# Kernel tuning notes

Hardware: AMD Instinct MI355X
Metric: run time of the kernel (lower is better)

## Reference

```python
import jax, jax.numpy as jnp
import numpy as np

N = 20000      # num nodes (num_words == num_sents, required by residual/linear reuse)
D = 128        # Dw == Ds (original code applies linear_word to both branches)
NE = 640000    # num edges
NEG_SLOPE = 0.2


def gat_conv(x, src, dst, W, a_src, a_dst, bias, num_nodes):
    """PyG GATConv, heads=1, concat=True. Edges are (src -> dst); softmax over
    incoming edges of each dst node."""
    h = x @ W                                   # (N, D_out)
    s_src = h @ a_src                           # (N,) att score per node as source
    s_dst = h @ a_dst                           # (N,) att score per node as target
    e = jax.nn.leaky_relu(s_src[src] + s_dst[dst], NEG_SLOPE)   # (E,)
    # segment softmax over dst
    emax = jax.ops.segment_max(e, dst, num_segments=num_nodes)  # (N,) -inf for empty ok
    ex = jnp.exp(e - emax[dst])                                  # (E,)
    denom = jax.ops.segment_sum(ex, dst, num_segments=num_nodes)
    alpha = ex / (denom[dst] + 1e-16)                            # (E,)
    out = jax.ops.segment_sum(alpha[:, None] * h[src], dst, num_segments=num_nodes)
    return out + bias


def setup_inputs() -> dict:
    key = jax.random.key(0)
    ks = jax.random.split(key, 12)
    Xw = jax.random.normal(ks[0], (N, D), dtype=jnp.float32)
    Xs = jax.random.normal(ks[1], (N, D), dtype=jnp.float32)
    edge_index = jax.random.randint(ks[2], (2, NE), 0, N)
    sc = 0.1
    return {
        "Xw": Xw,
        "Xs": Xs,
        "edge_index": edge_index,
        # gat_sent2word params (in=Ds, out=Dw)
        "W_s2w": jax.random.normal(ks[3], (D, D), dtype=jnp.float32) * sc,
        "a_src_s2w": jax.random.normal(ks[4], (D,), dtype=jnp.float32) * sc,
        "a_dst_s2w": jax.random.normal(ks[5], (D,), dtype=jnp.float32) * sc,
        "b_s2w": jnp.zeros((D,), dtype=jnp.float32),
        # gat_word2sent params (in=Dw, out=Ds)
        "W_w2s": jax.random.normal(ks[6], (D, D), dtype=jnp.float32) * sc,
        "a_src_w2s": jax.random.normal(ks[7], (D,), dtype=jnp.float32) * sc,
        "a_dst_w2s": jax.random.normal(ks[8], (D,), dtype=jnp.float32) * sc,
        "b_w2s": jnp.zeros((D,), dtype=jnp.float32),
        # linear_word (the original forward uses it for BOTH branches)
        "W_lin": jax.random.normal(ks[9], (D, D), dtype=jnp.float32) * sc,
        "b_lin": jnp.zeros((D,), dtype=jnp.float32),
    }


def reference(Xw, Xs, edge_index, W_s2w, a_src_s2w, a_dst_s2w, b_s2w,
              W_w2s, a_src_w2s, a_dst_w2s, b_w2s, W_lin, b_lin):
    num_nodes = Xw.shape[0]
    src, dst = edge_index[0], edge_index[1]
    # sent2word uses E as-is; word2sent uses Erev (flipped pairs)
    temp_word = gat_conv(Xs, src, dst, W_s2w, a_src_s2w, a_dst_s2w, b_s2w, num_nodes)
    temp_sent = gat_conv(Xw, dst, src, W_w2s, a_src_w2s, a_dst_w2s, b_w2s, num_nodes)
    hidden_word_next = (temp_word + Xw) @ W_lin + b_lin
    # NOTE: original code applies linear_word (not linear_sent) here — kept faithfully
    hidden_sent_next = (temp_sent + Xs) @ W_lin + b_lin
    return (hidden_word_next, hidden_sent_next)
```

## Files before the change

### kernel.cpp

```cpp
#include <hip/hip_runtime.h>
#include <hip/hip_bf16.h>
#include <stdint.h>

#define D 128
#define BKT_W 128
#define NB_MAX 256
#define RPB 128
#define CAPMAX 8192
#define EPT 8
#define FILL_T 512

typedef __attribute__((ext_vector_type(8))) short bf16x8;
typedef __attribute__((ext_vector_type(4))) float f32x4;

static __device__ __forceinline__ short f2bf(float x) {
    __hip_bfloat16 h = __float2bfloat16(x);
    return *reinterpret_cast<short*>(&h);
}

__global__ __launch_bounds__(256) void pack_w_k(const float* __restrict__ W0,
                                                const float* __restrict__ W1,
                                                const float* __restrict__ W2,
                                                short* __restrict__ P0,
                                                short* __restrict__ P1,
                                                short* __restrict__ P2,
                                                int* __restrict__ bcur, int nb2) {
    if (blockIdx.x == 0) {
        for (int i = threadIdx.x; i < nb2; i += 256) bcur[i] = 0;
    }
    int t = blockIdx.x * 256 + threadIdx.x;
    int m = t >> 11;
    int r = t & 2047;
    const float* W = (m == 0) ? W0 : (m == 1) ? W1 : W2;
    short*       P = (m == 0) ? P0 : (m == 1) ? P1 : P2;
    int lane = r & 63;
    int fr   = r >> 6;
    int kc = fr >> 3, ct = fr & 7;
    int col = ct * 16 + (lane & 15);
    int kb  = kc * 32 + 4 * (lane >> 4);
    short v[8];
#pragma unroll
    for (int e = 0; e < 8; ++e) {
        int k = kb + (e & 3) + 16 * (e >> 2);
        v[e] = f2bf(W[k * D + col]);
    }
    short* dst = P + (size_t)r * 8;
#pragma unroll
    for (int e = 0; e < 8; ++e) dst[e] = v[e];
}

__global__ __launch_bounds__(256) void fat_h_part_k(
    const float* __restrict__ IN0, const float* __restrict__ IN1,
    const short* __restrict__ P0,  const short* __restrict__ P1,
    short* __restrict__ HB0, short* __restrict__ HB1,
    const float* __restrict__ as0, const float* __restrict__ as1,
    const float* __restrict__ ad0, const float* __restrict__ ad1,
    float* __restrict__ ss0, float* __restrict__ ss1,
    float* __restrict__ sd0, float* __restrict__ sd1,
    int nrows, int mg,
    const int* __restrict__ esrc, const int* __restrict__ edst,
    int* __restrict__ bcur_d, int* __restrict__ bcur_s,
    uint32_t* __restrict__ rec_d, uint32_t* __restrict__ rec_s,
    int ne, int cap) {
    __shared__ __align__(16) char smem[RPB * 136 * 2 + 256];
    int bid = blockIdx.x;
    int tid = threadIdx.x;

    if (bid < 2 * mg) {
        int yy = (bid >= mg) ? 1 : 0;
        int xb = bid - yy * mg;
        const float* IN = yy ? IN1 : IN0;
        const short* PK = yy ? P1  : P0;
        short*       HB = yy ? HB1 : HB0;
        const float* a_src = yy ? as1 : as0;
        const float* a_dst = yy ? ad1 : ad0;
        float* ss = yy ? ss1 : ss0;
        float* sd = yy ? sd1 : sd0;
        short* As = (short*)smem;
        float* ps = (float*)(smem + RPB * 136 * 2);

        int row0 = xb * RPB;
        const float4* in4 = (const float4*)IN;
#pragma unroll
        for (int i = 0; i < 16; ++i) {
            int idx = tid + i * 256;
            int row = idx >> 5;
            int q   = idx & 31;
            float4 v = make_float4(0.f, 0.f, 0.f, 0.f);
            int grow = row0 + row;
            if (grow < nrows) v = in4[(size_t)grow * 32 + q];
            int kc = q >> 3, hi = (q >> 2) & 1, g2 = q & 3;
            short4 s4;
            s4.x = f2bf(v.x); s4.y = f2bf(v.y); s4.z = f2bf(v.z); s4.w = f2bf(v.w);
            *(short4*)&As[row * 136 + kc * 32 + g2 * 8 + hi * 4] = s4;
        }
        __syncthreads();

        int lane = tid & 63;
        int wv   = tid >> 6;
        const bf16x8* Wf = (const bf16x8*)PK;
        f32x4 acc[2][8] = {};
#pragma unroll
        for (int kc = 0; kc < 4; ++kc) {
            bf16x8 a0 = *(const bf16x8*)&As[(wv * 32 +      (lane & 15)) * 136 + kc * 32 + (lane >> 4) * 8];
            bf16x8 a1 = *(const bf16x8*)&As[(wv * 32 + 16 + (lane & 15)) * 136 + kc * 32 + (lane >> 4) * 8];
#pragma unroll
            for (int ct = 0; ct < 8; ++ct) {
                bf16x8 b = Wf[(kc * 8 + ct) * 64 + lane];
                acc[0][ct] = __builtin_amdgcn_mfma_f32_16x16x32_bf16(a0, b, acc[0][ct], 0, 0, 0);
                acc[1][ct] = __builtin_amdgcn_mfma_f32_16x16x32_bf16(a1, b, acc[1][ct], 0, 0, 0);
            }
        }

        int cb = lane & 15, rg = lane >> 4;
        float asv[8], adv[8];
#pragma unroll
        for (int ct = 0; ct < 8; ++ct) { asv[ct] = a_src[ct * 16 + cb]; adv[ct] = a_dst[ct * 16 + cb]; }
#pragma unroll
        for (int rt = 0; rt < 2; ++rt) {
            float ssum[4] = {0, 0, 0, 0}, dsum[4] = {0, 0, 0, 0};
#pragma unroll
            for (int ct = 0; ct < 8; ++ct) {
#pragma unroll
                for (int r = 0; r < 4; ++r) {
                    float x = acc[rt][ct][r];
                    int grow = row0 + wv * 32 + rt * 16 + rg * 4 + r;
                    if (grow < nrows) HB[(size_t)grow * D + ct * 16 + cb] = f2bf(x);
                    ssum[r] += x * asv[ct];
                    dsum[r] += x * adv[ct];
                }
            }
#pragma unroll
            for (int off = 1; off < 16; off <<= 1) {
#pragma unroll
                for (int r = 0; r < 4; ++r) {
                    ssum[r] += __shfl_xor(ssum[r], off);
                    dsum[r] += __shfl_xor(dsum[r], off);
                }
            }
            if (cb == 0) {
#pragma unroll
                for (int r = 0; r < 4; ++r) {
                    int grow = row0 + wv * 32 + rt * 16 + rg * 4 + r;
                    if (grow < nrows) {
                        ps[((rg * 2 + 0) * 8 + r) * 2 + 0] = 0.f;
                        ss[grow] = ssum[r]; sd[grow] = dsum[r];
                    }
                }
            }
        }
    } else {
        int pid = bid - 2 * mg;
        int* cnt  = (int*)smem;
        int* base = (int*)(smem + 2 * NB_MAX * 4);
        int blockStart = pid * 256 * EPT;
        for (int i = tid; i < 2 * NB_MAX; i += 256) cnt[i] = 0;
        __syncthreads();
        int s[EPT], d[EPT], sl_d[EPT], sl_s[EPT];
#pragma unroll
        for (int e = 0; e < EPT; ++e) {
            int i = blockStart + e * 256 + tid;
            s[e] = -1;
            if (i < ne) {
                s[e] = esrc[i]; d[e] = edst[i];
                sl_d[e] = atomicAdd(&cnt[0 * NB_MAX + (d[e] >> 7)], 1);
                sl_s[e] = atomicAdd(&cnt[1 * NB_MAX + (s[e] >> 7)], 1);
            }
        }
        __syncthreads();
        for (int i = tid; i < NB_MAX; i += 256) {
            if (cnt[0 * NB_MAX + i]) base[0 * NB_MAX + i] = atomicAdd(&bcur_d[i], cnt[0 * NB_MAX + i]);
            if (cnt[1 * NB_MAX + i]) base[1 * NB_MAX + i] = atomicAdd(&bcur_s[i], cnt[1 * NB_MAX + i]);
        }
        __syncthreads();
#pragma unroll
        for (int e = 0; e < EPT; ++e) {
            if (s[e] >= 0) {
                int bd = d[e] >> 7, bs = s[e] >> 7;
                int od = base[0 * NB_MAX + bd] + sl_d[e];
                int os = base[1 * NB_MAX + bs] + sl_s[e];
                if (od < cap) rec_d[(size_t)bd * cap + od] = (uint32_t)s[e] | ((uint32_t)(d[e] & 127) << 17);
                if (os < cap) rec_s[(size_t)bs * cap + os] = (uint32_t)d[e] | ((uint32_t)(s[e] & 127) << 17);
            }
        }
    }
}

__global__ __launch_bounds__(FILL_T) void csrfill_k(uint32_t* __restrict__ rec_d,
                                                    uint32_t* __restrict__ rec_s,
                                                    const int* __restrict__ bcur_d,
                                                    const int* __restrict__ bcur_s,
                                                    const float* __restrict__ ss1,
                                                    const float* __restrict__ sd1,
                                                    const float* __restrict__ ss2,
                                                    const float* __restrict__ sd2,
                                                    int2* __restrict__ nr_d,
                                                    int2* __restrict__ nr_s,
                                                    int n, int cap) {
    __shared__ uint32_t lrec[CAPMAX];
    __shared__ int deg[BKT_W], sbuf[BKT_W], cur[BKT_W];
    __shared__ float sdl[BKT_W];
    int dirv = blockIdx.y;
    uint32_t* rec   = dirv ? rec_s  : rec_d;
    const int* bc   = dirv ? bcur_s : bcur_d;
    const float* ss = dirv ? ss2 : ss1;
    const float* sv = dirv ? sd2 : sd1;
    int2* nr        = dirv ? nr_s : nr_d;
    int b = blockIdx.x, tid = threadIdx.x;
    int base = b * cap;
    int cnt = bc[b]; if (cnt > cap) cnt = cap;
    if (tid < BKT_W) {
        deg[tid] = 0;
        int node = b * BKT_W + tid;
        sdl[tid] = (node < n) ? sv[node] : 0.f;
    }
    for (int j = tid; j < cnt; j += FILL_T) lrec[j] = rec[base + j];
    __syncthreads();
    for (int j = tid; j < cnt; j += FILL_T) atomicAdd(&deg[lrec[j] >> 17], 1);
    __syncthreads();
    if (tid < BKT_W) sbuf[tid] = deg[tid];
    __syncthreads();
    for (int off = 1; off < BKT_W; off <<= 1) {
        int t = (tid < BKT_W && tid >= off) ? sbuf[tid - off] : 0;
        __syncthreads();
        if (tid < BKT_W) sbuf[tid] += t;
        __syncthreads();
    }
    if (tid < BKT_W) {
        int abs0 = base + sbuf[tid] - deg[tid];
        cur[tid] = abs0;
        int node = b * BKT_W + tid;
        if (node < n) nr[node] = make_int2(abs0, abs0 + deg[tid]);
    }
    __syncthreads();
    for (int j = tid; j < cnt; j += FILL_T) {
        uint32_t r = lrec[j];
        int g  = r >> 17;
        int nb = (int)(r & 0x1FFFFu);
        float e = ss[nb] + sdl[g];
        e = (e > 0.f) ? e : 0.2f * e;
        float w = __expf(e);
        rec[atomicAdd(&cur[g], 1)] = (((uint32_t)(unsigned short)f2bf(w)) << 16) | (uint32_t)nb;
    }
}

__global__ __launch_bounds__(256) void gat_gather_k(const int2* __restrict__ nr_d,
                                                    const int2* __restrict__ nr_s,
                                                    const uint32_t* __restrict__ erec_d,
                                                    const uint32_t* __restrict__ erec_s,
                                                    const short* __restrict__ hb1,
                                                    const short* __restrict__ hb2,
                                                    const float* __restrict__ b1,
                                                    const float* __restrict__ b2,
                                                    const float* __restrict__ Xw,
                                                    const float* __restrict__ Xs,
                                                    float* __restrict__ out, int n, int gB) {
    int bid = blockIdx.x;
    int dirv = (bid >= gB) ? 1 : 0;
    int xb = bid - dirv * gB;
    const int2*     nr   = dirv ? nr_s   : nr_d;
    const uint32_t* erec = dirv ? erec_s : erec_d;
    const short*    hb   = dirv ? hb2    : hb1;
    const float*    bias = dirv ? b2     : b1;
    const float*    resid= dirv ? Xs     : Xw;
    float*          outp = out + (size_t)dirv * n * D;

    int wave = (xb * 256 + (int)threadIdx.x) >> 6;
    int lane = threadIdx.x & 63;
    if (wave >= n) return;
    int2 be = nr[wave];
    int beg = be.x, end = be.y;
    int slot = lane >> 4;
    int c    = lane & 15;
    float acc[8] = {0, 0, 0, 0, 0, 0, 0, 0};
    float wsum = 0.f;
    for (int j = beg; j < end; j += 16) {
        uint32_t r[4];
#pragma unroll
        for (int u = 0; u < 4; ++u) {
            int i = j + 4 * u + slot;
            r[u] = (i < end) ? erec[i] : 0u;
        }
        uint4 h[4];
#pragma unroll
        for (int u = 0; u < 4; ++u)
            h[u] = *(const uint4*)(hb + (size_t)(r[u] & 0xFFFFu) * D + c * 8);
#pragma unroll
        for (int u = 0; u < 4; ++u) {
            float w = __uint_as_float(r[u] & 0xFFFF0000u);
            wsum += w;
            const uint32_t* pq = (const uint32_t*)&h[u];
#pragma unroll
            for (int q = 0; q < 4; ++q) {
                uint32_t a = pq[q];
                acc[2 * q]     += w * __uint_as_float(a << 16);
                acc[2 * q + 1] += w * __uint_as_float(a & 0xFFFF0000u);
            }
        }
    }
#pragma unroll
    for (int off = 16; off <= 32; off <<= 1) {
        wsum += __shfl_xor(wsum, off);
#pragma unroll
        for (int q = 0; q < 8; ++q) acc[q] += __shfl_xor(acc[q], off);
    }
    if (lane < 16) {
        float inv = 1.0f / (wsum + 1e-16f);
        size_t o = (size_t)wave * D + c * 8;
        float4 r0 = *(const float4*)(resid + o);
        float4 r1 = *(const float4*)(resid + o + 4);
        float4 o0, o1;
        o0.x = acc[0] * inv + bias[c * 8 + 0] + r0.x;
        o0.y = acc[1] * inv + bias[c * 8 + 1] + r0.y;
        o0.z = acc[2] * inv + bias[c * 8 + 2] + r0.z;
        o0.w = acc[3] * inv + bias[c * 8 + 3] + r0.w;
        o1.x = acc[4] * inv + bias[c * 8 + 4] + r1.x;
        o1.y = acc[5] * inv + bias[c * 8 + 5] + r1.y;
        o1.z = acc[6] * inv + bias[c * 8 + 6] + r1.z;
        o1.w = acc[7] * inv + bias[c * 8 + 7] + r1.w;
        *(float4*)(outp + o)     = o0;
        *(float4*)(outp + o + 4) = o1;
    }
}

__global__ __launch_bounds__(256) void mfma_ep_k(float* __restrict__ buf,
                                                 const short* __restrict__ PK,
                                                 const float* __restrict__ bias,
                                                 int nrows) {
    float* T = buf + (size_t)blockIdx.y * nrows * D;
    __shared__ short As[RPB * 136];
    int row0 = blockIdx.x * RPB;
    int tid  = threadIdx.x;
    const float4* in4 = (const float4*)T;
#pragma unroll
    for (int i = 0; i < 16; ++i) {
        int idx = tid + i * 256;
        int row = idx >> 5;
        int q   = idx & 31;
        float4 v = make_float4(0.f, 0.f, 0.f, 0.f);
        int grow = row0 + row;
        if (grow < nrows) v = in4[(size_t)grow * 32 + q];
        int kc = q >> 3, hi = (q >> 2) & 1, g2 = q & 3;
        short4 s4;
        s4.x = f2bf(v.x); s4.y = f2bf(v.y); s4.z = f2bf(v.z); s4.w = f2bf(v.w);
        *(short4*)&As[row * 136 + kc * 32 + g2 * 8 + hi * 4] = s4;
    }
    __syncthreads();

    int lane = tid & 63;
    int wv   = tid >> 6;
    const bf16x8* Wf = (const bf16x8*)PK;
    f32x4 acc[2][8] = {};
#pragma unroll
    for (int kc = 0; kc < 4; ++kc) {
        bf16x8 a0 = *(const bf16x8*)&As[(wv * 32 +      (lane & 15)) * 136 + kc * 32 + (lane >> 4) * 8];
        bf16x8 a1 = *(const bf16x8*)&As[(wv * 32 + 16 + (lane & 15)) * 136 + kc * 32 + (lane >> 4) * 8];
#pragma unroll
        for (int ct = 0; ct < 8; ++ct) {
            bf16x8 b = Wf[(kc * 8 + ct) * 64 + lane];
            acc[0][ct] = __builtin_amdgcn_mfma_f32_16x16x32_bf16(a0, b, acc[0][ct], 0, 0, 0);
            acc[1][ct] = __builtin_amdgcn_mfma_f32_16x16x32_bf16(a1, b, acc[1][ct], 0, 0, 0);
        }
    }

    int cb = lane & 15, rg = lane >> 4;
    float bv[8];
#pragma unroll
    for (int ct = 0; ct < 8; ++ct) bv[ct] = bias[ct * 16 + cb];
#pragma unroll
    for (int rt = 0; rt < 2; ++rt) {
#pragma unroll
        for (int ct = 0; ct < 8; ++ct) {
#pragma unroll
            for (int r = 0; r < 4; ++r) {
                int grow = row0 + wv * 32 + rt * 16 + rg * 4 + r;
                if (grow < nrows) T[(size_t)grow * D + ct * 16 + cb] = acc[rt][ct][r] + bv[ct];
            }
        }
    }
}

extern "C" void kernel_launch(void* const* d_in, const int* in_sizes, int n_in,
                              void* d_out, int out_size, void* d_ws, size_t ws_size,
                              hipStream_t stream) {
    const float* Xw    = (const float*)d_in[0];
    const float* Xs    = (const float*)d_in[1];
    const int*   edge  = (const int*)d_in[2];
    const float* W_s2w = (const float*)d_in[3];
    const float* as1   = (const float*)d_in[4];
    const float* ad1   = (const float*)d_in[5];
    const float* b1    = (const float*)d_in[6];
    const float* W_w2s = (const float*)d_in[7];
    const float* as2   = (const float*)d_in[8];
    const float* ad2   = (const float*)d_in[9];
    const float* b2    = (const float*)d_in[10];
    const float* W_lin = (const float*)d_in[11];
    const float* b_lin = (const float*)d_in[12];
    float* out = (float*)d_out;

    const int N  = in_sizes[0] / D;
    const int NE = in_sizes[2] / 2;
    const int NB = (N + BKT_W - 1) / BKT_W;
    int CAP = ((NE / NB) * 3 / 2 + 255) & ~255;
    if (CAP > CAPMAX) CAP = CAPMAX;
    const int* e_src = edge;
    const int* e_dst = edge + NE;

    char* p = (char*)d_ws;
    auto take = [&](size_t bytes) -> void* {
        p = (char*)(((uintptr_t)p + 255) & ~(uintptr_t)255);
        void* r = (void*)p;
        p += bytes;
        return r;
    };
    short* hb1  = (short*)take((size_t)N * D * 2);
    short* hb2  = (short*)take((size_t)N * D * 2);
    short* wpk1 = (short*)take((size_t)D * D * 2);
    short* wpk2 = (short*)take((size_t)D * D * 2);
    short* wpkL = (short*)take((size_t)D * D * 2);
    float* ss1  = (float*)take((size_t)N * 4);
    float* sd1  = (float*)take((size_t)N * 4);
    float* ss2  = (float*)take((size_t)N * 4);
    float* sd2  = (float*)take((size_t)N * 4);
    int*   bcur = (int*)take((size_t)2 * NB * 4);
    int*   bcur_d = bcur;
    int*   bcur_s = bcur + NB;
    int2*  nr_d = (int2*)take((size_t)N * 8);
    int2*  nr_s = (int2*)take((size_t)N * 8);
    uint32_t* rec_d = (uint32_t*)take((size_t)NB * CAP * 4);
    uint32_t* rec_s = (uint32_t*)take((size_t)NB * CAP * 4);

    pack_w_k<<<24, 256, 0, stream>>>(W_s2w, W_w2s, W_lin, wpk1, wpk2, wpkL, bcur, 2 * NB);

    int mg = (N + RPB - 1) / RPB;
    int partGrid = (NE + 256 * EPT - 1) / (256 * EPT);
    fat_h_part_k<<<2 * mg + partGrid, 256, 0, stream>>>(
        Xs, Xw, wpk1, wpk2, hb1, hb2,
        as1, as2, ad1, ad2, ss1, ss2, sd1, sd2, N, mg,
        e_src, e_dst, bcur_d, bcur_s, rec_d, rec_s, NE, CAP);

    dim3 fillGrid(NB, 2);
    csrfill_k<<<fillGrid, FILL_T, 0, stream>>>(rec_d, rec_s, bcur_d, bcur_s,
                                               ss1, sd1, ss2, sd2, nr_d, nr_s, N, CAP);

    int gB = (N + 3) / 4;
    gat_gather_k<<<2 * gB, 256, 0, stream>>>(nr_d, nr_s, rec_d, rec_s, hb1, hb2,
                                             b1, b2, Xw, Xs, out, N, gB);

    dim3 epGrid(mg, 2);
    mfma_ep_k<<<epGrid, 256, 0, stream>>>(out, wpkL, b_lin, N);
}
```

Measured before the change: 97.52 us.

## Fuse GAT gather with final linear MFMA epilogue and halve bucket width

Merges the neighbor-aggregation gather kernel and the separate MFMA linear epilogue into one kernel. Each 512-thread block aggregates 16 nodes into a bf16 tile in shared memory, then applies W_lin with MFMA and writes the final output. This removes one launch and a full fp32 intermediate write and re-read. The gather also prefetches up to 64 edge records per node with one coalesced load and spreads them by shuffle. Bucket width for the CSR build drops from 128 to 64 nodes, and a dead shared-memory store is removed. The cost is that each block issues only one 16-row MFMA per wave, and the blocks are larger.

```diff
diff --git a/kernel.cpp b/kernel.cpp
--- a/kernel.cpp
+++ b/kernel.cpp
@@ -3,10 +3,11 @@
 #include <stdint.h>
 
 #define D 128
-#define BKT_W 128
-#define NB_MAX 256
+#define BKT_W 64
+#define BKT_SH 6
+#define NB_MAX 512
 #define RPB 128
-#define CAPMAX 8192
+#define CAPMAX 4096
 #define EPT 8
 #define FILL_T 512
 
@@ -62,7 +63,7 @@
     int* __restrict__ bcur_d, int* __restrict__ bcur_s,
     uint32_t* __restrict__ rec_d, uint32_t* __restrict__ rec_s,
     int ne, int cap) {
-    __shared__ __align__(16) char smem[RPB * 136 * 2 + 256];
+    __shared__ __align__(16) char smem[RPB * 136 * 2];
     int bid = blockIdx.x;
     int tid = threadIdx.x;
 
@@ -77,7 +78,6 @@
         float* ss = yy ? ss1 : ss0;
         float* sd = yy ? sd1 : sd0;
         short* As = (short*)smem;
-        float* ps = (float*)(smem + RPB * 136 * 2);
 
         int row0 = xb * RPB;
         const float4* in4 = (const float4*)IN;
@@ -142,10 +142,7 @@
 #pragma unroll
                 for (int r = 0; r < 4; ++r) {
                     int grow = row0 + wv * 32 + rt * 16 + rg * 4 + r;
-                    if (grow < nrows) {
-                        ps[((rg * 2 + 0) * 8 + r) * 2 + 0] = 0.f;
-                        ss[grow] = ssum[r]; sd[grow] = dsum[r];
-                    }
+                    if (grow < nrows) { ss[grow] = ssum[r]; sd[grow] = dsum[r]; }
                 }
             }
         }
@@ -163,8 +160,8 @@
             s[e] = -1;
             if (i < ne) {
                 s[e] = esrc[i]; d[e] = edst[i];
-                sl_d[e] = atomicAdd(&cnt[0 * NB_MAX + (d[e] >> 7)], 1);
-                sl_s[e] = atomicAdd(&cnt[1 * NB_MAX + (s[e] >> 7)], 1);
+                sl_d[e] = atomicAdd(&cnt[0 * NB_MAX + (d[e] >> BKT_SH)], 1);
+                sl_s[e] = atomicAdd(&cnt[1 * NB_MAX + (s[e] >> BKT_SH)], 1);
             }
         }
         __syncthreads();
@@ -176,11 +173,11 @@
 #pragma unroll
         for (int e = 0; e < EPT; ++e) {
             if (s[e] >= 0) {
-                int bd = d[e] >> 7, bs = s[e] >> 7;
+                int bd = d[e] >> BKT_SH, bs = s[e] >> BKT_SH;
                 int od = base[0 * NB_MAX + bd] + sl_d[e];
                 int os = base[1 * NB_MAX + bs] + sl_s[e];
-                if (od < cap) rec_d[(size_t)bd * cap + od] = (uint32_t)s[e] | ((uint32_t)(d[e] & 127) << 17);
-                if (os < cap) rec_s[(size_t)bs * cap + os] = (uint32_t)d[e] | ((uint32_t)(s[e] & 127) << 17);
+                if (od < cap) rec_d[(size_t)bd * cap + od] = (uint32_t)s[e] | ((uint32_t)(d[e] & (BKT_W - 1)) << 17);
+                if (os < cap) rec_s[(size_t)bs * cap + os] = (uint32_t)d[e] | ((uint32_t)(s[e] & (BKT_W - 1)) << 17);
             }
         }
     }
@@ -244,17 +241,19 @@
     }
 }
 
-__global__ __launch_bounds__(256) void gat_gather_k(const int2* __restrict__ nr_d,
-                                                    const int2* __restrict__ nr_s,
-                                                    const uint32_t* __restrict__ erec_d,
-                                                    const uint32_t* __restrict__ erec_s,
-                                                    const short* __restrict__ hb1,
-                                                    const short* __restrict__ hb2,
-                                                    const float* __restrict__ b1,
-                                                    const float* __restrict__ b2,
-                                                    const float* __restrict__ Xw,
-                                                    const float* __restrict__ Xs,
-                                                    float* __restrict__ out, int n, int gB) {
+__global__ __launch_bounds__(512) void gat_ep_k(const int2* __restrict__ nr_d,
+                                                const int2* __restrict__ nr_s,
+                                                const uint32_t* __restrict__ erec_d,
+                                                const uint32_t* __restrict__ erec_s,
+                                                const short* __restrict__ hb1,
+                                                const short* __restrict__ hb2,
+                                                const float* __restrict__ b1,
+                                                const float* __restrict__ b2,
+                                                const float* __restrict__ Xw,
+                                                const float* __restrict__ Xs,
+                                                const short* __restrict__ wpkL,
+                                                const float* __restrict__ b_lin,
+                                                float* __restrict__ out, int n, int gB) {
     int bid = blockIdx.x;
     int dirv = (bid >= gB) ? 1 : 0;
     int xb = bid - dirv * gB;
@@ -265,118 +264,128 @@
     const float*    resid= dirv ? Xs     : Xw;
     float*          outp = out + (size_t)dirv * n * D;
 
-    int wave = (xb * 256 + (int)threadIdx.x) >> 6;
-    int lane = threadIdx.x & 63;
-    if (wave >= n) return;
-    int2 be = nr[wave];
-    int beg = be.x, end = be.y;
+    __shared__ short T[16 * 136];
+    int tid  = threadIdx.x;
+    int wv   = tid >> 6;
+    int lane = tid & 63;
     int slot = lane >> 4;
     int c    = lane & 15;
-    float acc[8] = {0, 0, 0, 0, 0, 0, 0, 0};
-    float wsum = 0.f;
-    for (int j = beg; j < end; j += 16) {
-        uint32_t r[4];
-#pragma unroll
-        for (int u = 0; u < 4; ++u) {
-            int i = j + 4 * u + slot;
-            r[u] = (i < end) ? erec[i] : 0u;
-        }
-        uint4 h[4];
-#pragma unroll
-        for (int u = 0; u < 4; ++u)
-            h[u] = *(const uint4*)(hb + (size_t)(r[u] & 0xFFFFu) * D + c * 8);
-#pragma unroll
-        for (int u = 0; u < 4; ++u) {
-            float w = __uint_as_float(r[u] & 0xFFFF0000u);
-            wsum += w;
-            const uint32_t* pq = (const uint32_t*)&h[u];
-#pragma unroll
-            for (int q = 0; q < 4; ++q) {
-                uint32_t a = pq[q];
-                acc[2 * q]     += w * __uint_as_float(a << 16);
-                acc[2 * q + 1] += w * __uint_as_float(a & 0xFFFF0000u);
-            }
-        }
-    }
-#pragma unroll
-    for (int off = 16; off <= 32; off <<= 1) {
-        wsum += __shfl_xor(wsum, off);
-#pragma unroll
-        for (int q = 0; q < 8; ++q) acc[q] += __shfl_xor(acc[q], off);
-    }
-    if (lane < 16) {
-        float inv = 1.0f / (wsum + 1e-16f);
-        size_t o = (size_t)wave * D + c * 8;
-        float4 r0 = *(const float4*)(resid + o);
-        float4 r1 = *(const float4*)(resid + o + 4);
-        float4 o0, o1;
-        o0.x = acc[0] * inv + bias[c * 8 + 0] + r0.x;
-        o0.y = acc[1] * inv + bias[c * 8 + 1] + r0.y;
-        o0.z = acc[2] * inv + bias[c * 8 + 2] + r0.z;
-        o0.w = acc[3] * inv + bias[c * 8 + 3] + r0.w;
-        o1.x = acc[4] * inv + bias[c * 8 + 4] + r1.x;
-        o1.y = acc[5] * inv + bias[c * 8 + 5] + r1.y;
-        o1.z = acc[6] * inv + bias[c * 8 + 6] + r1.z;
-        o1.w = acc[7] * inv + bias[c * 8 + 7] + r1.w;
-        *(float4*)(outp + o)     = o0;
-        *(float4*)(outp + o + 4) = o1;
-    }
-}
-
-__global__ __launch_bounds__(256) void mfma_ep_k(float* __restrict__ buf,
-                                                 const short* __restrict__ PK,
-                                                 const float* __restrict__ bias,
-                                                 int nrows) {
-    float* T = buf + (size_t)blockIdx.y * nrows * D;
-    __shared__ short As[RPB * 136];
-    int row0 = blockIdx.x * RPB;
-    int tid  = threadIdx.x;
-    const float4* in4 = (const float4*)T;
-#pragma unroll
-    for (int i = 0; i < 16; ++i) {
-        int idx = tid + i * 256;
-        int row = idx >> 5;
-        int q   = idx & 31;
-        float4 v = make_float4(0.f, 0.f, 0.f, 0.f);
-        int grow = row0 + row;
-        if (grow < nrows) v = in4[(size_t)grow * 32 + q];
-        int kc = q >> 3, hi = (q >> 2) & 1, g2 = q & 3;
-        short4 s4;
-        s4.x = f2bf(v.x); s4.y = f2bf(v.y); s4.z = f2bf(v.z); s4.w = f2bf(v.w);
-        *(short4*)&As[row * 136 + kc * 32 + g2 * 8 + hi * 4] = s4;
+    int nbase = xb * 16;
+
+#pragma unroll
+    for (int h = 0; h < 2; ++h) {
+        int node = nbase + wv * 2 + h;
+        int lrow = wv * 2 + h;
+        float acc[8] = {0, 0, 0, 0, 0, 0, 0, 0};
+        float wsum = 0.f;
+        bool valid = (node < n);
+        if (valid) {
+            int2 be = nr[node];
+            int beg = be.x, end = be.y;
+            int deg = end - beg;
+            uint32_t rpre = 0;
+            if (lane < deg) rpre = erec[beg + lane];
+            int nfull = (deg < 64) ? deg : 64;
+            for (int jj = 0; jj < nfull; jj += 16) {
+                uint32_t r[4];
+#pragma unroll
+                for (int u = 0; u < 4; ++u)
+                    r[u] = (uint32_t)__shfl((int)rpre, jj + 4 * u + slot);
+                uint4 hrow[4];
+#pragma unroll
+                for (int u = 0; u < 4; ++u)
+                    hrow[u] = *(const uint4*)(hb + (size_t)(r[u] & 0xFFFFu) * D + c * 8);
+#pragma unroll
+                for (int u = 0; u < 4; ++u) {
+                    float w = __uint_as_float(r[u] & 0xFFFF0000u);
+                    wsum += w;
+                    const uint32_t* pq = (const uint32_t*)&hrow[u];
+#pragma unroll
+                    for (int q = 0; q < 4; ++q) {
+                        uint32_t a = pq[q];
+                        acc[2 * q]     += w * __uint_as_float(a << 16);
+                        acc[2 * q + 1] += w * __uint_as_float(a & 0xFFFF0000u);
+                    }
+                }
+            }
+            for (int j = beg + 64; j < end; j += 16) {
+                uint32_t r[4];
+#pragma unroll
+                for (int u = 0; u < 4; ++u) {
+                    int i = j + 4 * u + slot;
+                    r[u] = (i < end) ? erec[i] : 0u;
+                }
+#pragma unroll
+                for (int u = 0; u < 4; ++u) {
+                    uint4 hrow = *(const uint4*)(hb + (size_t)(r[u] & 0xFFFFu) * D + c * 8);
+                    float w = __uint_as_float(r[u] & 0xFFFF0000u);
+                    wsum += w;
+                    const uint32_t* pq = (const uint32_t*)&hrow;
+#pragma unroll
+                    for (int q = 0; q < 4; ++q) {
+                        uint32_t a = pq[q];
+                        acc[2 * q]     += w * __uint_as_float(a << 16);
+                        acc[2 * q + 1] += w * __uint_as_float(a & 0xFFFF0000u);
+                    }
+                }
+            }
+        }
+#pragma unroll
+        for (int off = 16; off <= 32; off <<= 1) {
+            wsum += __shfl_xor(wsum, off);
+#pragma unroll
+            for (int q = 0; q < 8; ++q) acc[q] += __shfl_xor(acc[q], off);
+        }
+        if (lane < 16) {
+            float v[8];
+            if (valid) {
+                float inv = 1.0f / (wsum + 1e-16f);
+                size_t o = (size_t)node * D + lane * 8;
+                float4 r0 = *(const float4*)(resid + o);
+                float4 r1 = *(const float4*)(resid + o + 4);
+                float4 bb0 = *(const float4*)(bias + lane * 8);
+                float4 bb1 = *(const float4*)(bias + lane * 8 + 4);
+                v[0] = acc[0] * inv + bb0.x + r0.x;
+                v[1] = acc[1] * inv + bb0.y + r0.y;
+                v[2] = acc[2] * inv + bb0.z + r0.z;
+                v[3] = acc[3] * inv + bb0.w + r0.w;
+                v[4] = acc[4] * inv + bb1.x + r1.x;
+                v[5] = acc[5] * inv + bb1.y + r1.y;
+                v[6] = acc[6] * inv + bb1.z + r1.z;
+                v[7] = acc[7] * inv + bb1.w + r1.w;
+            } else {
+#pragma unroll
+                for (int m = 0; m < 8; ++m) v[m] = 0.f;
+            }
+#pragma unroll
+            for (int half = 0; half < 2; ++half) {
+                int k0 = lane * 8 + half * 4;
+                int kc = k0 >> 5, hi = (k0 >> 4) & 1, g2 = (k0 >> 2) & 3;
+                short4 s4;
+                s4.x = f2bf(v[half * 4 + 0]);
+                s4.y = f2bf(v[half * 4 + 1]);
+                s4.z = f2bf(v[half * 4 + 2]);
+                s4.w = f2bf(v[half * 4 + 3]);
+                *(short4*)&T[lrow * 136 + kc * 32 + g2 * 8 + hi * 4] = s4;
+            }
+        }
     }
     __syncthreads();
 
-    int lane = tid & 63;
-    int wv   = tid >> 6;
-    const bf16x8* Wf = (const bf16x8*)PK;
-    f32x4 acc[2][8] = {};
+    const bf16x8* Wf = (const bf16x8*)wpkL;
+    f32x4 acc2 = {};
 #pragma unroll
     for (int kc = 0; kc < 4; ++kc) {
-        bf16x8 a0 = *(const bf16x8*)&As[(wv * 32 +      (lane & 15)) * 136 + kc * 32 + (lane >> 4) * 8];
-        bf16x8 a1 = *(const bf16x8*)&As[(wv * 32 + 16 + (lane & 15)) * 136 + kc * 32 + (lane >> 4) * 8];
-#pragma unroll
-        for (int ct = 0; ct < 8; ++ct) {
-            bf16x8 b = Wf[(kc * 8 + ct) * 64 + lane];
-            acc[0][ct] = __builtin_amdgcn_mfma_f32_16x16x32_bf16(a0, b, acc[0][ct], 0, 0, 0);
-            acc[1][ct] = __builtin_amdgcn_mfma_f32_16x16x32_bf16(a1, b, acc[1][ct], 0, 0, 0);
-        }
-    }
-
+        bf16x8 a = *(const bf16x8*)&T[(lane & 15) * 136 + kc * 32 + (lane >> 4) * 8];
+        bf16x8 b = Wf[(kc * 8 + wv) * 64 + lane];
+        acc2 = __builtin_amdgcn_mfma_f32_16x16x32_bf16(a, b, acc2, 0, 0, 0);
+    }
     int cb = lane & 15, rg = lane >> 4;
-    float bv[8];
-#pragma unroll
-    for (int ct = 0; ct < 8; ++ct) bv[ct] = bias[ct * 16 + cb];
-#pragma unroll
-    for (int rt = 0; rt < 2; ++rt) {
-#pragma unroll
-        for (int ct = 0; ct < 8; ++ct) {
-#pragma unroll
-            for (int r = 0; r < 4; ++r) {
-                int grow = row0 + wv * 32 + rt * 16 + rg * 4 + r;
-                if (grow < nrows) T[(size_t)grow * D + ct * 16 + cb] = acc[rt][ct][r] + bv[ct];
-            }
-        }
+    float bv = b_lin[wv * 16 + cb];
+#pragma unroll
+    for (int r = 0; r < 4; ++r) {
+        int grow = nbase + rg * 4 + r;
+        if (grow < n) outp[(size_t)grow * D + wv * 16 + cb] = acc2[r] + bv;
     }
 }
 
@@ -443,10 +452,7 @@
     csrfill_k<<<fillGrid, FILL_T, 0, stream>>>(rec_d, rec_s, bcur_d, bcur_s,
                                                ss1, sd1, ss2, sd2, nr_d, nr_s, N, CAP);
 
-    int gB = (N + 3) / 4;
-    gat_gather_k<<<2 * gB, 256, 0, stream>>>(nr_d, nr_s, rec_d, rec_s, hb1, hb2,
-                                             b1, b2, Xw, Xs, out, N, gB);
-
-    dim3 epGrid(mg, 2);
-    mfma_ep_k<<<epGrid, 256, 0, stream>>>(out, wpkL, b_lin, N);
-}
+    int gB = (N + 15) / 16;
+    gat_ep_k<<<2 * gB, 512, 0, stream>>>(nr_d, nr_s, rec_d, rec_s, hb1, hb2,
+                                         b1, b2, Xw, Xs, wpkL, b_lin, out, N, gB);
+}
```

Result: faster. 86.69 us (-11.1%).
